# Kernel tuning notes

Measured on AMD Instinct MI355X. Metric: run time of the kernel, lower is better.

The kernel has to match this reference:

```python
import jax, jax.numpy as jnp
import numpy as np

DIM = 768
N_HEADS = 12
HEAD_DIM = DIM // N_HEADS
B, S = 2, 4096


def setup_inputs() -> dict:
    key = jax.random.key(0)
    k_x, k_wqkv, k_bqkv, k_wout, k_bout = jax.random.split(key, 5)
    scale_in = 1.0 / np.sqrt(DIM)
    return {
        "x": jax.random.normal(k_x, (B, S, DIM), dtype=jnp.float32),
        "Wqkv": jax.random.normal(k_wqkv, (DIM, 3 * DIM), dtype=jnp.float32) * scale_in,
        "bqkv": jax.random.normal(k_bqkv, (3 * DIM,), dtype=jnp.float32) * 0.02,
        "Wout": jax.random.normal(k_wout, (DIM, DIM), dtype=jnp.float32) * scale_in,
        "bout": jax.random.normal(k_bout, (DIM,), dtype=jnp.float32) * 0.02,
    }


def reference(x, Wqkv, bqkv, Wout, bout):
    b, s, d = x.shape
    qkv = (x @ Wqkv + bqkv).reshape(b, s, 3, N_HEADS, HEAD_DIM)
    qkv = jnp.transpose(qkv, (2, 0, 3, 1, 4))  # [3, B, H, S, hd]
    q, k, v = qkv[0], qkv[1], qkv[2]
    scale = HEAD_DIM ** -0.5
    attn = jnp.einsum('bhqd,bhkd->bhqk', q, k) * scale  # [B, H, S, S]
    causal_mask = jnp.triu(jnp.ones((s, s), dtype=bool), k=1)
    attn = jnp.where(causal_mask[None, None], -jnp.inf, attn)
    attn = jax.nn.softmax(attn, axis=-1)
    out = jnp.einsum('bhqk,bhkd->bhqd', attn, v)  # [B, H, S, hd]
    out = jnp.transpose(out, (0, 2, 1, 3)).reshape(b, s, d)
    return out @ Wout + bout
```

## Files before the change

### kernel.cpp

```cpp
#include <hip/hip_runtime.h>
#include <hip/hip_bf16.h>
#include <math.h>

#define DIM 768
#define NH 12
#define HD 64
#define BATCH 2
#define SEQ 4096
#define MTOT (BATCH * SEQ)

#define QSCALE 0.1803368801111244f

typedef unsigned short u16;
typedef __bf16 bf16x8 __attribute__((ext_vector_type(8)));
typedef float  f32x4  __attribute__((ext_vector_type(4)));
typedef float  f32x16 __attribute__((ext_vector_type(16)));
typedef unsigned short u16x4 __attribute__((ext_vector_type(4)));
typedef unsigned short u16x8 __attribute__((ext_vector_type(8)));
typedef unsigned u32x4 __attribute__((ext_vector_type(4)));

__device__ inline u16 f2bf(float f) {
    unsigned u = __builtin_bit_cast(unsigned, f);
    u += 0x7fffu + ((u >> 16) & 1u);
    return (u16)(u >> 16);
}

#if defined(__has_builtin) && __has_builtin(__builtin_amdgcn_cvt_pk_bf16_f32)
#define HAVE_PK_BF16 1
__device__ inline unsigned pk2bf(float a, float b) {
    auto v = __builtin_amdgcn_cvt_pk_bf16_f32(a, b);
    return __builtin_bit_cast(unsigned, v);
}
#else
#define HAVE_PK_BF16 0
__device__ inline unsigned pk2bf(float a, float b) {
    return (unsigned)f2bf(a) | ((unsigned)f2bf(b) << 16);
}
#endif

__device__ inline f32x16 mfma32(bf16x8 a, bf16x8 b, f32x16 c) {
    return __builtin_amdgcn_mfma_f32_32x32x16_bf16(a, b, c, 0, 0, 0);
}

__device__ inline void gl2lds16(const u16* g, u16* l) {
    __builtin_amdgcn_global_load_lds(
        (const __attribute__((address_space(1))) void*)g,
        (__attribute__((address_space(3))) void*)l,
        16, 0, 0);
}

__global__ __launch_bounds__(256)
void cvt_bf16(const float* __restrict__ src, u16* __restrict__ dst, int n8)
{
    int i = blockIdx.x * 256 + threadIdx.x;
    if (i >= n8) return;
    float4 a = ((const float4*)src)[i * 2];
    float4 b = ((const float4*)src)[i * 2 + 1];
    u16x8 o;
    o[0] = f2bf(a.x); o[1] = f2bf(a.y); o[2] = f2bf(a.z); o[3] = f2bf(a.w);
    o[4] = f2bf(b.x); o[5] = f2bf(b.y); o[6] = f2bf(b.z); o[7] = f2bf(b.w);
    ((u16x8*)dst)[i] = o;
}

__global__ __launch_bounds__(256)
void transpose_to_bf16(const float* __restrict__ src, u16* __restrict__ dst,
                       int R, int C)
{
    __shared__ float tile[32][33];
    const int c0 = blockIdx.x * 32, r0 = blockIdx.y * 32;
    const int tx = threadIdx.x & 31, ty = threadIdx.x >> 5;
#pragma unroll
    for (int i = 0; i < 4; ++i) {
        int row = ty * 4 + i;
        tile[row][tx] = src[(size_t)(r0 + row) * C + c0 + tx];
    }
    __syncthreads();
#pragma unroll
    for (int i = 0; i < 4; ++i) {
        int crow = ty * 4 + i;
        dst[(size_t)(c0 + crow) * R + r0 + tx] = f2bf(tile[tx][crow]);
    }
}

__device__ inline void gemm_lds_mainloop(const u16* __restrict__ Ag,
                                         const u16* __restrict__ Bg,
                                         int m0, int n0, int w, int lane,
                                         u16 (*As)[64 * 64], u16 (*Bs)[64 * 64],
                                         f32x16 acc[2][2])
{
    const int lc32 = lane & 31, hi = lane >> 5;
    const int wm = (w & 1) * 64, wn = (w >> 1) * 64;
    const int drow = lane >> 3;
    const int dp   = lane & 7;

#pragma unroll
    for (int mi = 0; mi < 2; ++mi)
#pragma unroll
        for (int nj = 0; nj < 2; ++nj)
            acc[mi][nj] = f32x16{};

#pragma unroll
    for (int i = 0; i < 2; ++i) {
        const int r  = w * 16 + i * 8 + drow;
        const int g  = dp ^ (r & 7);
        const int tr = 2 * r + (g >> 2);
        const int kc = g & 3;
        gl2lds16(Ag + (size_t)(m0 + tr) * 768 + kc * 8, &As[0][(w * 16 + i * 8) * 64]);
        gl2lds16(Bg + (size_t)(n0 + tr) * 768 + kc * 8, &Bs[0][(w * 16 + i * 8) * 64]);
    }
    __syncthreads();

    for (int ks = 0; ks < 24; ++ks) {
        const int cur = ks & 1;

        if (ks < 23) {
            const int k0n = (ks + 1) * 32;
#pragma unroll
            for (int i = 0; i < 2; ++i) {
                const int r  = w * 16 + i * 8 + drow;
                const int g  = dp ^ (r & 7);
                const int tr = 2 * r + (g >> 2);
                const int kc = g & 3;
                gl2lds16(Ag + (size_t)(m0 + tr) * 768 + k0n + kc * 8,
                         &As[1 - cur][(w * 16 + i * 8) * 64]);
                gl2lds16(Bg + (size_t)(n0 + tr) * 768 + k0n + kc * 8,
                         &Bs[1 - cur][(w * 16 + i * 8) * 64]);
            }
        }

        bf16x8 af[2][2], bfr[2][2];
#pragma unroll
        for (int mi = 0; mi < 2; ++mi)
#pragma unroll
            for (int kh = 0; kh < 2; ++kh) {
                const int m = wm + mi * 32 + lc32;
                const int r = m >> 1;
                const int p = ((m & 1) * 4 + kh * 2 + hi) ^ (r & 7);
                af[mi][kh] = *(const bf16x8*)&As[cur][r * 64 + p * 8];
            }
#pragma unroll
        for (int nj = 0; nj < 2; ++nj)
#pragma unroll
            for (int kh = 0; kh < 2; ++kh) {
                const int n = wn + nj * 32 + lc32;
                const int r = n >> 1;
                const int p = ((n & 1) * 4 + kh * 2 + hi) ^ (r & 7);
                bfr[nj][kh] = *(const bf16x8*)&Bs[cur][r * 64 + p * 8];
            }

        __builtin_amdgcn_s_setprio(1);
#pragma unroll
        for (int mi = 0; mi < 2; ++mi)
#pragma unroll
            for (int nj = 0; nj < 2; ++nj) {
                acc[mi][nj] = mfma32(af[mi][0], bfr[nj][0], acc[mi][nj]);
                acc[mi][nj] = mfma32(af[mi][1], bfr[nj][1], acc[mi][nj]);
            }
        __builtin_amdgcn_s_setprio(0);

        __syncthreads();
    }
}

__global__ __launch_bounds__(256, 4)
void gemm_qkv_mfma(const u16* __restrict__ A, const u16* __restrict__ Bt,
                   const float* __restrict__ bias,
                   u16* __restrict__ Qb, u16* __restrict__ Kb, u16* __restrict__ Vt)
{
    __shared__ u16 As[2][64 * 64];
    __shared__ u16 Bs[2][64 * 64];
    const int m0 = blockIdx.x * 128;
    const int n0 = blockIdx.y * 128;
    const int t = threadIdx.x;
    const int w = t >> 6, lane = t & 63;
    const int lc32 = lane & 31, hi = lane >> 5;
    const int wm = (w & 1) * 64, wn = (w >> 1) * 64;

    f32x16 acc[2][2];
    gemm_lds_mainloop(A, Bt, m0, n0, w, lane, As, Bs, acc);

    const int b  = m0 >> 12;
    const int s0 = (m0 & 4095) + wm;
    const int nbase = n0 + wn;
    const int three = nbase / 768;
    const int rem   = nbase - three * 768;
    const int h     = rem >> 6;
    const int bh    = b * NH + h;

    if (three < 2) {
        u16* dst = (three == 0) ? Qb : Kb;
        const float qs = (three == 0) ? QSCALE : 1.0f;
#pragma unroll
        for (int nj = 0; nj < 2; ++nj) {
            const int d = nj * 32 + lc32;
            const float bi = bias[nbase + d];
#pragma unroll
            for (int mi = 0; mi < 2; ++mi)
#pragma unroll
                for (int r = 0; r < 16; ++r) {
                    const int s = s0 + mi * 32 + (r & 3) + 8 * (r >> 2) + 4 * hi;
                    dst[((size_t)bh * SEQ + s) * HD + d] = f2bf((acc[mi][nj][r] + bi) * qs);
                }
        }
    } else {
#pragma unroll
        for (int nj = 0; nj < 2; ++nj) {
            const int d = nj * 32 + lc32;
            const float bi = bias[nbase + d];
            const size_t rowb = ((size_t)bh * HD + d) * SEQ;
#pragma unroll
            for (int mi = 0; mi < 2; ++mi)
#pragma unroll
                for (int g = 0; g < 4; ++g) {
                    const int s = s0 + mi * 32 + 8 * g + 4 * hi;
                    u16x4 wv;
#pragma unroll
                    for (int rr = 0; rr < 4; ++rr)
                        wv[rr] = f2bf(acc[mi][nj][g * 4 + rr] + bi);
                    *(u16x4*)&Vt[rowb + s] = wv;
                }
        }
    }
}

__global__ __launch_bounds__(256, 4)
void gemm_out_mfma(const u16* __restrict__ A, const u16* __restrict__ Bt,
                   const float* __restrict__ bias, float* __restrict__ C)
{
    __shared__ u16 As[2][64 * 64];
    __shared__ u16 Bs[2][64 * 64];
    const int m0 = blockIdx.x * 128;
    const int n0 = blockIdx.y * 128;
    const int t = threadIdx.x;
    const int w = t >> 6, lane = t & 63;
    const int lc32 = lane & 31, hi = lane >> 5;
    const int wm = (w & 1) * 64, wn = (w >> 1) * 64;

    f32x16 acc[2][2];
    gemm_lds_mainloop(A, Bt, m0, n0, w, lane, As, Bs, acc);

#pragma unroll
    for (int nj = 0; nj < 2; ++nj) {
        const int col = n0 + wn + nj * 32 + lc32;
        const float bi = bias[col];
#pragma unroll
        for (int mi = 0; mi < 2; ++mi)
#pragma unroll
            for (int r = 0; r < 16; ++r) {
                const int row = m0 + wm + mi * 32 + (r & 3) + 8 * (r >> 2) + 4 * hi;
                C[(size_t)row * 768 + col] = acc[mi][nj][r] + bi;
            }
    }
}

__global__ __launch_bounds__(256, 4)
void flash_attn(const u16* __restrict__ Qg, const u16* __restrict__ Kg,
                const u16* __restrict__ Vtg, u16* __restrict__ Og)
{
    const int bh   = blockIdx.x;
    const int qt   = 63 - (int)blockIdx.y;
    const int b    = bh / NH, h = bh % NH;
    const int t    = threadIdx.x;
    const int w    = t >> 6;
    const int wq   = w >> 1;
    const int wk   = w & 1;
    const int lane = t & 63;
    const int lc32 = lane & 31;
    const int hi   = lane >> 5;
    const int drow = lane >> 3;
    const int dp   = lane & 7;

    __shared__ u16 Ks[2][64 * 64];
    __shared__ u16 Vs[2][64 * 64];

    const u16* Qp = Qg  + (size_t)bh * SEQ * HD;
    const u16* Kp = Kg  + (size_t)bh * SEQ * HD;
    const u16* Vp = Vtg + (size_t)bh * HD * SEQ;
    float* Vscr = (float*)&Vs[0][0];
    float* Lx   = (float*)&Ks[0][0];

    const int qrow0 = qt * 64 + wq * 32;

    bf16x8 qa[4];
#pragma unroll
    for (int ds = 0; ds < 4; ++ds)
        qa[ds] = *(const bf16x8*)
            &Qp[(size_t)(qrow0 + lc32) * HD + ds * 16 + hi * 8];

    f32x16 o2[2];
    o2[0] = f32x16{};
    o2[1] = f32x16{};
    float l_r = 0.f;

#pragma unroll
    for (int i = 0; i < 2; ++i) {
        const int r0  = w * 16 + i * 8;
        const int row = r0 + drow;
        const int gc  = dp ^ (row & 7);
        gl2lds16(Kp + (size_t)row * HD + gc * 8, &Ks[0][r0 * 64]);
        gl2lds16(Vp + (size_t)row * SEQ + gc * 8, &Vs[0][r0 * 64]);
    }
    __syncthreads();

    for (int tk = 0; tk <= qt; ++tk) {
        const int kb  = tk * 64;
        const int cur = tk & 1;

        if (tk < qt) {
            const int kbn = kb + 64;
#pragma unroll
            for (int i = 0; i < 2; ++i) {
                const int r0  = w * 16 + i * 8;
                const int row = r0 + drow;
                const int gc  = dp ^ (row & 7);
                gl2lds16(Kp + (size_t)(kbn + row) * HD + gc * 8,
                         &Ks[1 - cur][r0 * 64]);
                gl2lds16(Vp + (size_t)row * SEQ + kbn + gc * 8,
                         &Vs[1 - cur][r0 * 64]);
            }
        }

        f32x16 sacc = {};
        {
            const int row = wk * 32 + lc32;
            const int sw  = row & 7;
            __builtin_amdgcn_s_setprio(1);
#pragma unroll
            for (int ds = 0; ds < 4; ++ds) {
                bf16x8 kf = *(const bf16x8*)
                    &Ks[cur][row * 64 + (((ds * 2 + hi) ^ sw) * 8)];
                sacc = mfma32(kf, qa[ds], sacc);
            }
            __builtin_amdgcn_s_setprio(0);
        }

        if (tk == qt) {
            const int q = qrow0 + lc32;
#pragma unroll
            for (int r = 0; r < 16; ++r) {
                const int key = kb + wk * 32 + (r & 3) + 8 * (r >> 2) + 4 * hi;
                if (key > q) sacc[r] = -1e30f;
            }
        }

        float pv[16];
#pragma unroll
        for (int r = 0; r < 16; ++r)
            pv[r] = __builtin_amdgcn_exp2f(sacc[r]);

        l_r += (((pv[0] + pv[1]) + (pv[2] + pv[3]))
              + ((pv[4] + pv[5]) + (pv[6] + pv[7])))
             + (((pv[8] + pv[9]) + (pv[10] + pv[11]))
              + ((pv[12] + pv[13]) + (pv[14] + pv[15])));

        bf16x8 pa[2];
#pragma unroll
        for (int s = 0; s < 2; ++s) {
            unsigned w0 = pk2bf(pv[8 * s + 0], pv[8 * s + 1]);
            unsigned w1 = pk2bf(pv[8 * s + 2], pv[8 * s + 3]);
            unsigned w2 = pk2bf(pv[8 * s + 4], pv[8 * s + 5]);
            unsigned w3 = pk2bf(pv[8 * s + 6], pv[8 * s + 7]);
            asm("v_permlane32_swap_b32 %0, %1" : "+v"(w0), "+v"(w2));
            asm("v_permlane32_swap_b32 %0, %1" : "+v"(w1), "+v"(w3));
            u32x4 tw;
            tw[0] = w0; tw[1] = w1; tw[2] = w2; tw[3] = w3;
            pa[s] = __builtin_bit_cast(bf16x8, tw);
        }

        __builtin_amdgcn_s_setprio(1);
#pragma unroll
        for (int dt = 0; dt < 2; ++dt) {
            const int row = dt * 32 + lc32;
            const int sw  = row & 7;
#pragma unroll
            for (int s = 0; s < 2; ++s) {
                bf16x8 vf = *(const bf16x8*)
                    &Vs[cur][row * 64 + (((wk * 4 + s * 2 + hi) ^ sw) * 8)];
                o2[dt] = mfma32(pa[s], vf, o2[dt]);
            }
        }
        __builtin_amdgcn_s_setprio(0);

        __syncthreads();
    }

    const float lt = l_r + __shfl_xor(l_r, 32);

    if (wk == 1) {
#pragma unroll
        for (int dt = 0; dt < 2; ++dt)
#pragma unroll
            for (int r = 0; r < 16; ++r) {
                const int ql = (r & 3) + 8 * (r >> 2) + 4 * hi;
                Vscr[wq * 2048 + ql * 64 + dt * 32 + lc32] = o2[dt][r];
            }
        if (lane < 32) Lx[wq * 32 + lc32] = lt;
    }
    __syncthreads();
    if (wk == 0) {
        const float linv_q = 1.0f / (lt + Lx[wq * 32 + lc32]);
#pragma unroll
        for (int r = 0; r < 16; ++r) {
            const int ql   = (r & 3) + 8 * (r >> 2) + 4 * hi;
            const float li = __shfl(linv_q, ql);
            const int q = qrow0 + ql;
            const size_t base = ((size_t)(b * SEQ + q)) * DIM + h * HD + lc32;
#pragma unroll
            for (int dt = 0; dt < 2; ++dt) {
                const float ov = o2[dt][r]
                    + Vscr[wq * 2048 + ql * 64 + dt * 32 + lc32];
                Og[base + dt * 32] = f2bf(ov * li);
            }
        }
    }
}

extern "C" void kernel_launch(void* const* d_in, const int* in_sizes, int n_in,
                              void* d_out, int out_size, void* d_ws, size_t ws_size,
                              hipStream_t stream)
{
    const float* x    = (const float*)d_in[0];
    const float* Wqkv = (const float*)d_in[1];
    const float* bqkv = (const float*)d_in[2];
    const float* Wout = (const float*)d_in[3];
    const float* bout = (const float*)d_in[4];
    float* out = (float*)d_out;

    const size_t NX  = (size_t)MTOT * DIM;
    const size_t NWQ = (size_t)DIM * 3 * DIM;
    const size_t NWO = (size_t)DIM * DIM;
    u16* p   = (u16*)d_ws;
    u16* Xb  = p;              p += NX;
    u16* Wqt = p;              p += NWQ;
    u16* Wot = p;              p += NWO;
    u16* Qb  = p;              p += NX;
    u16* Kb  = p;              p += NX;
    u16* Vt  = p;              p += NX;
    u16* Ao  = p;

    cvt_bf16<<<(int)(NX / 8 + 255) / 256, 256, 0, stream>>>(x, Xb, (int)(NX / 8));
    transpose_to_bf16<<<dim3(2304 / 32, 768 / 32), 256, 0, stream>>>(Wqkv, Wqt, 768, 2304);
    transpose_to_bf16<<<dim3(768 / 32, 768 / 32), 256, 0, stream>>>(Wout, Wot, 768, 768);

    gemm_qkv_mfma<<<dim3(MTOT / 128, 2304 / 128), 256, 0, stream>>>(Xb, Wqt, bqkv, Qb, Kb, Vt);
    flash_attn<<<dim3(24, 64), 256, 0, stream>>>(Qb, Kb, Vt, Ao);
    gemm_out_mfma<<<dim3(MTOT / 128, 768 / 128), 256, 0, stream>>>(Ao, Wot, bout, out);
}
```

Measured before the change: 240.5 us.

## Triple-buffer GEMM LDS tiles with vmcnt waits and a single barrier

Moves the projection GEMM mainloop from double to triple buffering in LDS, issuing loads two k-steps ahead. Each iteration waits with a partial s_waitcnt vmcnt and does one barrier in place of the trailing __syncthreads. The aim is to hide global-to-LDS latency and drop one barrier per step. In exchange the LDS footprint grows by half and launch bounds fall to 3 blocks per SM, which may cut occupancy.

```diff
diff --git a/kernel.cpp b/kernel.cpp
--- a/kernel.cpp
+++ b/kernel.cpp
@@ -99,32 +99,42 @@
         for (int nj = 0; nj < 2; ++nj)
             acc[mi][nj] = f32x16{};
 
+    int trA[2], kcA[2], lr0[2];
 #pragma unroll
     for (int i = 0; i < 2; ++i) {
-        const int r  = w * 16 + i * 8 + drow;
-        const int g  = dp ^ (r & 7);
-        const int tr = 2 * r + (g >> 2);
-        const int kc = g & 3;
-        gl2lds16(Ag + (size_t)(m0 + tr) * 768 + kc * 8, &As[0][(w * 16 + i * 8) * 64]);
-        gl2lds16(Bg + (size_t)(n0 + tr) * 768 + kc * 8, &Bs[0][(w * 16 + i * 8) * 64]);
-    }
-    __syncthreads();
-
+        const int r = w * 16 + i * 8 + drow;
+        const int g = dp ^ (r & 7);
+        trA[i] = 2 * r + (g >> 2);
+        kcA[i] = g & 3;
+        lr0[i] = (w * 16 + i * 8) * 64;
+    }
+
+#pragma unroll
+    for (int i = 0; i < 2; ++i) {
+        gl2lds16(Ag + (size_t)(m0 + trA[i]) * 768 + kcA[i] * 8, &As[0][lr0[i]]);
+        gl2lds16(Bg + (size_t)(n0 + trA[i]) * 768 + kcA[i] * 8, &Bs[0][lr0[i]]);
+    }
+#pragma unroll
+    for (int i = 0; i < 2; ++i) {
+        gl2lds16(Ag + (size_t)(m0 + trA[i]) * 768 + 32 + kcA[i] * 8, &As[1][lr0[i]]);
+        gl2lds16(Bg + (size_t)(n0 + trA[i]) * 768 + 32 + kcA[i] * 8, &Bs[1][lr0[i]]);
+    }
+
+    int cur = 0;
     for (int ks = 0; ks < 24; ++ks) {
-        const int cur = ks & 1;
-
-        if (ks < 23) {
-            const int k0n = (ks + 1) * 32;
+        if (ks + 1 < 24) { asm volatile("s_waitcnt vmcnt(4)" ::: "memory"); }
+        else             { asm volatile("s_waitcnt vmcnt(0)" ::: "memory"); }
+        __builtin_amdgcn_s_barrier();
+
+        if (ks + 2 < 24) {
+            const int nb = (cur >= 1) ? (cur - 1) : 2;
+            const int k0 = (ks + 2) * 32;
 #pragma unroll
             for (int i = 0; i < 2; ++i) {
-                const int r  = w * 16 + i * 8 + drow;
-                const int g  = dp ^ (r & 7);
-                const int tr = 2 * r + (g >> 2);
-                const int kc = g & 3;
-                gl2lds16(Ag + (size_t)(m0 + tr) * 768 + k0n + kc * 8,
-                         &As[1 - cur][(w * 16 + i * 8) * 64]);
-                gl2lds16(Bg + (size_t)(n0 + tr) * 768 + k0n + kc * 8,
-                         &Bs[1 - cur][(w * 16 + i * 8) * 64]);
+                gl2lds16(Ag + (size_t)(m0 + trA[i]) * 768 + k0 + kcA[i] * 8,
+                         &As[nb][lr0[i]]);
+                gl2lds16(Bg + (size_t)(n0 + trA[i]) * 768 + k0 + kcA[i] * 8,
+                         &Bs[nb][lr0[i]]);
             }
         }
 
@@ -158,17 +168,17 @@
             }
         __builtin_amdgcn_s_setprio(0);
 
-        __syncthreads();
-    }
-}
-
-__global__ __launch_bounds__(256, 4)
+        cur = (cur == 2) ? 0 : cur + 1;
+    }
+}
+
+__global__ __launch_bounds__(256, 3)
 void gemm_qkv_mfma(const u16* __restrict__ A, const u16* __restrict__ Bt,
                    const float* __restrict__ bias,
                    u16* __restrict__ Qb, u16* __restrict__ Kb, u16* __restrict__ Vt)
 {
-    __shared__ u16 As[2][64 * 64];
-    __shared__ u16 Bs[2][64 * 64];
+    __shared__ u16 As[3][64 * 64];
+    __shared__ u16 Bs[3][64 * 64];
     const int m0 = blockIdx.x * 128;
     const int n0 = blockIdx.y * 128;
     const int t = threadIdx.x;
@@ -223,12 +233,12 @@
     }
 }
 
-__global__ __launch_bounds__(256, 4)
+__global__ __launch_bounds__(256, 3)
 void gemm_out_mfma(const u16* __restrict__ A, const u16* __restrict__ Bt,
                    const float* __restrict__ bias, float* __restrict__ C)
 {
-    __shared__ u16 As[2][64 * 64];
-    __shared__ u16 Bs[2][64 * 64];
+    __shared__ u16 As[3][64 * 64];
+    __shared__ u16 Bs[3][64 * 64];
     const int m0 = blockIdx.x * 128;
     const int n0 = blockIdx.y * 128;
     const int t = threadIdx.x;
```

Result: faster. 235.6 us (-2.0%).
